# Optimization experiments

Measured on AMD Instinct MI355X. Metric: run time of the kernel, lower is better.

The kernel has to match this reference:

```python
import jax, jax.numpy as jnp
import numpy as np

EMBED_DIM = 512
NUM_HEADS = 8
HEAD_DIM = EMBED_DIM // NUM_HEADS
GRID = 48
BATCH = 8


def _locality_bias(grid_h, grid_w):
    # normalised negative squared L2 distances between patch centres, in [-1, 0]
    gy, gx = jnp.meshgrid(jnp.linspace(0.0, 1.0, grid_h),
                          jnp.linspace(0.0, 1.0, grid_w), indexing='ij')
    coords = jnp.stack([gy.reshape(-1), gx.reshape(-1)], axis=-1)  # (N, 2)
    diff = coords[None, :, :] - coords[:, None, :]                 # (N, N, 2)
    dist2 = jnp.sum(diff * diff, axis=-1)                          # (N, N)
    return -dist2 / jnp.max(dist2)


def setup_inputs() -> dict:
    key = jax.random.key(0)
    k_x, k_qkv, k_pw, k_pb, k_t, k_lw = jax.random.split(key, 6)
    N = GRID * GRID
    x = jax.random.normal(k_x, (BATCH, N, EMBED_DIM), dtype=jnp.float32)
    # torch nn.Linear weights are (out_features, in_features)
    qkv_w = jax.random.normal(k_qkv, (3 * EMBED_DIM, EMBED_DIM), dtype=jnp.float32) * 0.02
    proj_w = jax.random.normal(k_pw, (EMBED_DIM, EMBED_DIM), dtype=jnp.float32) * 0.02
    proj_b = jax.random.normal(k_pb, (EMBED_DIM,), dtype=jnp.float32) * 0.02
    init_temp = float(np.log(HEAD_DIM ** (-0.5)))
    temperature = init_temp + 0.02 * jax.random.normal(k_t, (NUM_HEADS, 1, 1), dtype=jnp.float32)
    locality_weight = 0.1 + 0.02 * jax.random.normal(k_lw, (NUM_HEADS,), dtype=jnp.float32)
    return {
        'x': x,
        'qkv_w': qkv_w,
        'proj_w': proj_w,
        'proj_b': proj_b,
        'temperature': temperature,
        'locality_weight': locality_weight,
        'grid_h': GRID,
        'grid_w': GRID,
    }


def reference(x, qkv_w, proj_w, proj_b, temperature, locality_weight, grid_h, grid_w):
    B, N, C = x.shape
    H = temperature.shape[0]
    D = C // H
    # qkv projection (no bias): (B, N, 3C) -> (3, B, H, N, D)
    qkv = (x @ qkv_w.T).reshape(B, N, 3, H, D)
    qkv = jnp.transpose(qkv, (2, 0, 3, 1, 4))
    q, k, v = qkv[0], qkv[1], qkv[2]              # each (B, H, N, D)
    scale = jnp.exp(temperature)                  # (H, 1, 1) learnable per-head temp
    attn = jnp.einsum('bhqd,bhkd->bhqk', q, k) * scale[None]
    loc = _locality_bias(grid_h, grid_w)          # (N, N), values in [-1, 0]
    attn = attn + locality_weight[None, :, None, None] * loc[None, None]
    attn = jax.nn.softmax(attn, axis=-1)          # dropout is identity (p=0 / eval)
    out = jnp.einsum('bhqk,bhkd->bhqd', attn, v)  # (B, H, N, D)
    out = jnp.transpose(out, (0, 2, 1, 3)).reshape(B, N, C)
    return out @ proj_w.T + proj_b
```

## Files before the change

### kernel.cpp

```cpp
#include <hip/hip_runtime.h>

typedef unsigned int   uint_ma   __attribute__((may_alias));
typedef unsigned short ushort_ma __attribute__((may_alias));
typedef float          float_ma  __attribute__((may_alias));
typedef __bf16 bf16x8 __attribute__((ext_vector_type(8)));
typedef float f32x4 __attribute__((ext_vector_type(4)));
typedef uint_ma u32x4 __attribute__((ext_vector_type(4)));
typedef ushort_ma u16x4 __attribute__((ext_vector_type(4)));

#define BATCH 8
#define NTOK 2304
#define CDIM 512
#define NH 8
#define HD 64
#define MROWS (BATCH * NTOK)
#define LOG2E 1.44269504088896f

constexpr size_t N_X  = (size_t)BATCH * NTOK * CDIM;
constexpr size_t N_WQ = (size_t)3 * CDIM * CDIM;
constexpr size_t N_WP = (size_t)CDIM * CDIM;
constexpr size_t OFF_XO = 0;
constexpr size_t OFF_WQ = OFF_XO + N_X;
constexpr size_t OFF_WP = OFF_WQ + N_WQ;
constexpr size_t OFF_Q  = OFF_WP + N_WP;
constexpr size_t OFF_K  = OFF_Q + N_X;
constexpr size_t OFF_V  = OFF_K + N_X;
constexpr size_t CV8 = (N_X + N_WQ + N_WP) / 8;

__device__ __forceinline__ float bf2f(unsigned short h) {
  unsigned int u = ((unsigned int)h) << 16;
  return __builtin_bit_cast(float, u);
}
__device__ __forceinline__ unsigned short f2bf(float f) {
  unsigned int u = __builtin_bit_cast(unsigned int, f);
  u += 0x7fffu + ((u >> 16) & 1u);
  return (unsigned short)(u >> 16);
}

__global__ __launch_bounds__(256) void convert3(
    const float* __restrict__ s0, const float* __restrict__ s1,
    const float* __restrict__ s2, ushort_ma* __restrict__ base) {
  const size_t gid = (size_t)blockIdx.x * blockDim.x + threadIdx.x;
  const size_t stride = (size_t)gridDim.x * blockDim.x;
  for (size_t i = gid; i < CV8; i += stride) {
    size_t r = i;
    const float* src;
    size_t doff;
    if (r < N_X / 8) { src = s0; doff = OFF_XO; }
    else if ((r -= N_X / 8) < N_WQ / 8) { src = s1; doff = OFF_WQ; }
    else { r -= N_WQ / 8; src = s2; doff = OFF_WP; }
    const f32x4* fw = (const f32x4*)(src + r * 8);
    const f32x4 a = fw[0], b = fw[1];
    u16x4 lo, hi;
#pragma unroll
    for (int j = 0; j < 4; j++) { lo[j] = f2bf(a[j]); hi[j] = f2bf(b[j]); }
    ushort_ma* dst = base + doff + r * 8;
    *(u16x4*)dst = lo;
    *(u16x4*)(dst + 4) = hi;
  }
}

template <int MODE>
__global__ __launch_bounds__(256, 2) void gemm_bt(
    const ushort_ma* __restrict__ A, const ushort_ma* __restrict__ W,
    const float* __restrict__ aux,
    unsigned short* __restrict__ o0,
    unsigned short* __restrict__ o1,
    unsigned short* __restrict__ o2)
{
  __shared__ __align__(16) ushort_ma As[128][40];
  __shared__ __align__(16) ushort_ma Bs[128][40];
  const int K = CDIM;
  const int m0 = blockIdx.x * 128;
  const int n0 = blockIdx.y * 128;
  const int t = threadIdx.x;
  const int lane = t & 63;
  const int w = t >> 6;
  const int wm = (w >> 1) * 64, wn = (w & 1) * 64;
  const int lr = lane & 15, lq = lane >> 4;

  const int ra = t >> 2;
  const int sa = (t & 3) * 8;
  const ushort_ma* Ag = A + (size_t)(m0 + ra) * K + sa;
  const ushort_ma* Ag2 = Ag + (size_t)64 * K;
  const ushort_ma* Bg = W + (size_t)(n0 + ra) * K + sa;
  const ushort_ma* Bg2 = Bg + (size_t)64 * K;

  const f32x4 fz = {0.f, 0.f, 0.f, 0.f};
  f32x4 acc[4][4];
#pragma unroll
  for (int i = 0; i < 4; i++)
#pragma unroll
    for (int j = 0; j < 4; j++) acc[i][j] = fz;

  u32x4 pa = *(const u32x4*)(Ag);
  u32x4 pa2 = *(const u32x4*)(Ag2);
  u32x4 pb = *(const u32x4*)(Bg);
  u32x4 pb2 = *(const u32x4*)(Bg2);

  for (int kt = 0; kt < 16; kt++) {
    __syncthreads();
    *(u32x4*)(&As[ra][sa]) = pa;
    *(u32x4*)(&As[ra + 64][sa]) = pa2;
    *(u32x4*)(&Bs[ra][sa]) = pb;
    *(u32x4*)(&Bs[ra + 64][sa]) = pb2;
    __syncthreads();
    if (kt < 15) {
      const int k0 = (kt + 1) * 32;
      pa = *(const u32x4*)(Ag + k0);
      pa2 = *(const u32x4*)(Ag2 + k0);
      pb = *(const u32x4*)(Bg + k0);
      pb2 = *(const u32x4*)(Bg2 + k0);
    }
    bf16x8 af[4], bfr[4];
#pragma unroll
    for (int i = 0; i < 4; i++)
      af[i] = __builtin_bit_cast(bf16x8, *(const u32x4*)(&As[wm + i * 16 + lr][lq * 8]));
#pragma unroll
    for (int j = 0; j < 4; j++)
      bfr[j] = __builtin_bit_cast(bf16x8, *(const u32x4*)(&Bs[wn + j * 16 + lr][lq * 8]));
#pragma unroll
    for (int i = 0; i < 4; i++)
#pragma unroll
      for (int j = 0; j < 4; j++)
        acc[i][j] = __builtin_amdgcn_mfma_f32_16x16x32_bf16(af[i], bfr[j], acc[i][j], 0, 0, 0);
  }

  if (MODE == 0) {
#pragma unroll
    for (int j = 0; j < 4; j++) {
      const int gc = n0 + wn + j * 16 + lr;
      const int which = gc >> 9;
      const int h = (gc >> 6) & 7;
      const int d = gc & 63;
#pragma unroll
      for (int i = 0; i < 4; i++) {
        const int gm0 = m0 + wm + i * 16 + lq * 4;
        const int b = gm0 / NTOK;
        const int np = gm0 - b * NTOK;
        if (which == 2) {
          u16x4 pk;
#pragma unroll
          for (int r = 0; r < 4; r++) pk[r] = f2bf(acc[i][j][r]);
          *(u16x4*)(o2 + ((size_t)((b * NH + h) * HD + d)) * NTOK + np) = pk;
        } else {
          const float sc = (which == 0) ? __expf(aux[h]) * LOG2E : 1.0f;
          unsigned short* dst = (which == 0) ? o0 : o1;
          const size_t base = ((size_t)((b * NH + h) * NTOK + np)) * HD + d;
#pragma unroll
          for (int r = 0; r < 4; r++) dst[base + (size_t)r * HD] = f2bf(acc[i][j][r] * sc);
        }
      }
    }
  } else {
    float_ma* outf = (float_ma*)o0;
#pragma unroll
    for (int j = 0; j < 4; j++) {
      const int gc = n0 + wn + j * 16 + lr;
      const float bv = aux[gc];
#pragma unroll
      for (int i = 0; i < 4; i++) {
        const int gm0 = m0 + wm + i * 16 + lq * 4;
#pragma unroll
        for (int r = 0; r < 4; r++)
          outf[(size_t)(gm0 + r) * CDIM + gc] = acc[i][j][r] + bv;
      }
    }
  }
}

__global__ __launch_bounds__(256, 3) void attn_kernel(
    const ushort_ma* __restrict__ Qg,
    const ushort_ma* __restrict__ Kg,
    const ushort_ma* __restrict__ Vg,
    const float* __restrict__ lwp,
    unsigned short* __restrict__ Og)
{
  __shared__ __align__(16) ushort_ma Ks[128][72];
  __shared__ __align__(16) ushort_ma Vs[64][136];
  __shared__ __align__(16) ushort_ma Ps[4][32][40];

  const int bh = blockIdx.y;
  const int b = bh >> 3, h = bh & 7;
  const int q0 = blockIdx.x * 128;
  const int t = threadIdx.x;
  const int lane = t & 63;
  const int w = t >> 6;
  const int lr = lane & 15, lq = lane >> 4;

  {
    const ushort_ma* Qb = Qg + ((size_t)bh * NTOK + q0) * HD;
#pragma unroll
    for (int it = 0; it < 4; it++) {
      const int q = t + it * 256;
      const int row = q >> 3, seg = (q & 7) * 8;
      *(u32x4*)(&Ks[row][seg]) = *(const u32x4*)(Qb + (size_t)row * HD + seg);
    }
  }
  __syncthreads();
  bf16x8 aQ[2][2];
#pragma unroll
  for (int mi = 0; mi < 2; mi++)
#pragma unroll
    for (int ks = 0; ks < 2; ks++)
      aQ[mi][ks] = __builtin_bit_cast(
          bf16x8, *(const u32x4*)(&Ks[w * 32 + mi * 16 + lr][ks * 32 + lq * 8]));

  const float cb2 = -0.5f * LOG2E * lwp[h];
  float cc[8], dd[8];
#pragma unroll
  for (int mi = 0; mi < 2; mi++)
#pragma unroll
    for (int r = 0; r < 4; r++) {
      const int qi = q0 + w * 32 + mi * 16 + lq * 4 + r;
      const int yy = qi / 48;
      const int xx = qi - yy * 48;
      cc[mi * 4 + r] = -2.0f * cb2 * ((float)yy * (1.0f / 47.0f));
      dd[mi * 4 + r] = -2.0f * cb2 * ((float)xx * (1.0f / 47.0f));
    }

  float l_i[8];
#pragma unroll
  for (int i = 0; i < 8; i++) l_i[i] = 0.0f;
  const f32x4 fz = {0.f, 0.f, 0.f, 0.f};
  f32x4 accO[2][4];
#pragma unroll
  for (int mi = 0; mi < 2; mi++)
#pragma unroll
    for (int nd = 0; nd < 4; nd++) accO[mi][nd] = fz;

  const ushort_ma* Kb = Kg + (size_t)bh * NTOK * HD;
  const ushort_ma* Vb = Vg + (size_t)bh * HD * NTOK;

  for (int kt = 0; kt < 18; kt++) {
    const int kv0 = kt * 128;
    __syncthreads();
    u32x4 kc[4], vc[4];
#pragma unroll
    for (int it = 0; it < 4; it++) {
      const int q = t + it * 256;
      kc[it] = *(const u32x4*)(Kb + (size_t)(kv0 + (q >> 3)) * HD + (q & 7) * 8);
      vc[it] = *(const u32x4*)(Vb + (size_t)(q >> 4) * NTOK + kv0 + (q & 15) * 8);
    }
#pragma unroll
    for (int it = 0; it < 4; it++) {
      const int q = t + it * 256;
      *(u32x4*)(&Ks[q >> 3][(q & 7) * 8]) = kc[it];
      *(u32x4*)(&Vs[q >> 4][(q & 15) * 8]) = vc[it];
    }
    __syncthreads();

    float ky[8], kx[8], be8[8];
#pragma unroll
    for (int ni = 0; ni < 8; ni++) {
      const int kj = kv0 + ni * 16 + lr;
      const int yy = kj / 48;
      const int xx = kj - yy * 48;
      const float fy = (float)yy * (1.0f / 47.0f);
      const float fx = (float)xx * (1.0f / 47.0f);
      ky[ni] = fy;
      kx[ni] = fx;
      be8[ni] = fmaf(cb2, fmaf(fy, fy, fx * fx), -8.0f);
    }

#pragma unroll
    for (int c = 0; c < 4; c++) {
      f32x4 s2[2][2] = {{fz, fz}, {fz, fz}};
#pragma unroll
      for (int e2 = 0; e2 < 2; e2++) {
        const int ni = 2 * c + e2;
#pragma unroll
        for (int ks = 0; ks < 2; ks++) {
          const bf16x8 bK = __builtin_bit_cast(
              bf16x8, *(const u32x4*)(&Ks[ni * 16 + lr][ks * 32 + lq * 8]));
#pragma unroll
          for (int mi = 0; mi < 2; mi++)
            s2[mi][e2] = __builtin_amdgcn_mfma_f32_16x16x32_bf16(aQ[mi][ks], bK, s2[mi][e2], 0, 0, 0);
        }
      }
#pragma unroll
      for (int e2 = 0; e2 < 2; e2++) {
        const int ni = 2 * c + e2;
        const float kyv = ky[ni], kxv = kx[ni], bev = be8[ni];
#pragma unroll
        for (int mi = 0; mi < 2; mi++)
#pragma unroll
          for (int r = 0; r < 4; r++) {
            const int ri = mi * 4 + r;
            float v = s2[mi][e2][r] + bev;
            v = fmaf(cc[ri], kyv, v);
            v = fmaf(dd[ri], kxv, v);
            const float p = __builtin_amdgcn_exp2f(v);
            const unsigned int pu = __builtin_bit_cast(unsigned int, p);
            l_i[ri] += __builtin_bit_cast(float, pu & 0xffff0000u);
            Ps[w][mi * 16 + lq * 4 + r][e2 * 16 + lr] = (unsigned short)(pu >> 16);
          }
      }
      __asm__ volatile("s_waitcnt lgkmcnt(0)" ::: "memory");
      bf16x8 aP[2];
#pragma unroll
      for (int mi = 0; mi < 2; mi++)
        aP[mi] = __builtin_bit_cast(
            bf16x8, *(const u32x4*)(&Ps[w][mi * 16 + lr][lq * 8]));
#pragma unroll
      for (int nd = 0; nd < 4; nd++) {
        const bf16x8 bV = __builtin_bit_cast(
            bf16x8, *(const u32x4*)(&Vs[nd * 16 + lr][c * 32 + lq * 8]));
#pragma unroll
        for (int mi = 0; mi < 2; mi++)
          accO[mi][nd] = __builtin_amdgcn_mfma_f32_16x16x32_bf16(aP[mi], bV, accO[mi][nd], 0, 0, 0);
      }
    }
  }

#pragma unroll
  for (int ri = 0; ri < 8; ri++) {
    float lv = l_i[ri];
    lv += __shfl_xor(lv, 1);
    lv += __shfl_xor(lv, 2);
    lv += __shfl_xor(lv, 4);
    lv += __shfl_xor(lv, 8);
    l_i[ri] = 1.0f / lv;
  }
#pragma unroll
  for (int mi = 0; mi < 2; mi++)
#pragma unroll
    for (int nd = 0; nd < 4; nd++)
#pragma unroll
      for (int r = 0; r < 4; r++) {
        const int np = q0 + w * 32 + mi * 16 + lq * 4 + r;
        Og[((size_t)(b * NTOK + np)) * CDIM + h * HD + nd * 16 + lr] =
            f2bf(accO[mi][nd][r] * l_i[mi * 4 + r]);
      }
}

extern "C" void kernel_launch(void* const* d_in, const int* in_sizes, int n_in,
                              void* d_out, int out_size, void* d_ws, size_t ws_size,
                              hipStream_t stream) {
  const float* x      = (const float*)d_in[0];
  const float* qkv_w  = (const float*)d_in[1];
  const float* proj_w = (const float*)d_in[2];
  const float* proj_b = (const float*)d_in[3];
  const float* temp   = (const float*)d_in[4];
  const float* lw     = (const float*)d_in[5];

  ushort_ma* base = (ushort_ma*)d_ws;
  ushort_ma* XB  = base + OFF_XO;
  ushort_ma* WQB = base + OFF_WQ;
  ushort_ma* WPB = base + OFF_WP;
  ushort_ma* Q   = base + OFF_Q;
  ushort_ma* Kt  = base + OFF_K;
  ushort_ma* Vt  = base + OFF_V;
  ushort_ma* O   = XB;

  convert3<<<1024, 256, 0, stream>>>(x, qkv_w, proj_w, base);
  gemm_bt<0><<<dim3(MROWS / 128, 1536 / 128), 256, 0, stream>>>(
      XB, WQB, temp, (unsigned short*)Q, (unsigned short*)Kt, (unsigned short*)Vt);
  attn_kernel<<<dim3(NTOK / 128, BATCH * NH), 256, 0, stream>>>(
      Q, Kt, Vt, lw, (unsigned short*)O);
  gemm_bt<1><<<dim3(MROWS / 128, CDIM / 128), 256, 0, stream>>>(
      O, WPB, proj_b, (unsigned short*)d_out, nullptr, nullptr);
}
```

Before: 326.0 us.

## Fold locality bias into score MFMA and use async LDS loads in GEMM

```diff
diff --git a/kernel.cpp b/kernel.cpp
--- a/kernel.cpp
+++ b/kernel.cpp
@@ -35,6 +35,12 @@
   unsigned int u = __builtin_bit_cast(unsigned int, f);
   u += 0x7fffu + ((u >> 16) & 1u);
   return (unsigned short)(u >> 16);
+}
+
+__device__ __forceinline__ void gload16(const void* g, void* l) {
+  __builtin_amdgcn_global_load_lds(
+      (const __attribute__((address_space(1))) void*)g,
+      (__attribute__((address_space(3))) void*)l, 16, 0, 0);
 }
 
 __global__ __launch_bounds__(256) void convert3(
@@ -68,8 +74,8 @@
     unsigned short* __restrict__ o1,
     unsigned short* __restrict__ o2)
 {
-  __shared__ __align__(16) ushort_ma As[128][40];
-  __shared__ __align__(16) ushort_ma Bs[128][40];
+  __shared__ __align__(16) ushort_ma As[2][128][32];
+  __shared__ __align__(16) ushort_ma Bs[2][128][32];
   const int K = CDIM;
   const int m0 = blockIdx.x * 128;
   const int n0 = blockIdx.y * 128;
@@ -79,12 +85,12 @@
   const int wm = (w >> 1) * 64, wn = (w & 1) * 64;
   const int lr = lane & 15, lq = lane >> 4;
 
-  const int ra = t >> 2;
-  const int sa = (t & 3) * 8;
-  const ushort_ma* Ag = A + (size_t)(m0 + ra) * K + sa;
-  const ushort_ma* Ag2 = Ag + (size_t)64 * K;
-  const ushort_ma* Bg = W + (size_t)(n0 + ra) * K + sa;
-  const ushort_ma* Bg2 = Bg + (size_t)64 * K;
+  const int srow = w * 16 + (lane >> 2);
+  const int scg = (lane & 3) ^ ((srow >> 1) & 3);
+  const ushort_ma* Ag0 = A + (size_t)(m0 + srow) * K + scg * 8;
+  const ushort_ma* Ag1 = Ag0 + (size_t)64 * K;
+  const ushort_ma* Bg0 = W + (size_t)(n0 + srow) * K + scg * 8;
+  const ushort_ma* Bg1 = Bg0 + (size_t)64 * K;
 
   const f32x4 fz = {0.f, 0.f, 0.f, 0.f};
   f32x4 acc[4][4];
@@ -93,32 +99,28 @@
 #pragma unroll
     for (int j = 0; j < 4; j++) acc[i][j] = fz;
 
-  u32x4 pa = *(const u32x4*)(Ag);
-  u32x4 pa2 = *(const u32x4*)(Ag2);
-  u32x4 pb = *(const u32x4*)(Bg);
-  u32x4 pb2 = *(const u32x4*)(Bg2);
+  auto issue = [&](int kt, int buf) {
+    const int k0 = kt * 32;
+    gload16(Ag0 + k0, (void*)&As[buf][w * 16][0]);
+    gload16(Ag1 + k0, (void*)&As[buf][64 + w * 16][0]);
+    gload16(Bg0 + k0, (void*)&Bs[buf][w * 16][0]);
+    gload16(Bg1 + k0, (void*)&Bs[buf][64 + w * 16][0]);
+  };
+
+  issue(0, 0);
+  const int colf = 8 * (lq ^ ((lr >> 1) & 3));
 
   for (int kt = 0; kt < 16; kt++) {
+    const int buf = kt & 1;
     __syncthreads();
-    *(u32x4*)(&As[ra][sa]) = pa;
-    *(u32x4*)(&As[ra + 64][sa]) = pa2;
-    *(u32x4*)(&Bs[ra][sa]) = pb;
-    *(u32x4*)(&Bs[ra + 64][sa]) = pb2;
-    __syncthreads();
-    if (kt < 15) {
-      const int k0 = (kt + 1) * 32;
-      pa = *(const u32x4*)(Ag + k0);
-      pa2 = *(const u32x4*)(Ag2 + k0);
-      pb = *(const u32x4*)(Bg + k0);
-      pb2 = *(const u32x4*)(Bg2 + k0);
-    }
+    if (kt < 15) issue(kt + 1, buf ^ 1);
     bf16x8 af[4], bfr[4];
 #pragma unroll
     for (int i = 0; i < 4; i++)
-      af[i] = __builtin_bit_cast(bf16x8, *(const u32x4*)(&As[wm + i * 16 + lr][lq * 8]));
+      af[i] = __builtin_bit_cast(bf16x8, *(const u32x4*)(&As[buf][wm + i * 16 + lr][colf]));
 #pragma unroll
     for (int j = 0; j < 4; j++)
-      bfr[j] = __builtin_bit_cast(bf16x8, *(const u32x4*)(&Bs[wn + j * 16 + lr][lq * 8]));
+      bfr[j] = __builtin_bit_cast(bf16x8, *(const u32x4*)(&Bs[buf][wn + j * 16 + lr][colf]));
 #pragma unroll
     for (int i = 0; i < 4; i++)
 #pragma unroll
@@ -176,7 +178,7 @@
     const float* __restrict__ lwp,
     unsigned short* __restrict__ Og)
 {
-  __shared__ __align__(16) ushort_ma Ks[128][72];
+  __shared__ __align__(16) ushort_ma Ks[128][96];
   __shared__ __align__(16) ushort_ma Vs[64][136];
   __shared__ __align__(16) ushort_ma Ps[4][32][40];
 
@@ -188,6 +190,12 @@
   const int w = t >> 6;
   const int lr = lane & 15, lq = lane >> 4;
 
+  if (t < 128) {
+    const u32x4 z4 = {0u, 0u, 0u, 0u};
+    *(u32x4*)(&Ks[t][72]) = z4;
+    *(u32x4*)(&Ks[t][80]) = z4;
+    *(u32x4*)(&Ks[t][88]) = z4;
+  }
   {
     const ushort_ma* Qb = Qg + ((size_t)bh * NTOK + q0) * HD;
 #pragma unroll
@@ -207,17 +215,21 @@
           bf16x8, *(const u32x4*)(&Ks[w * 32 + mi * 16 + lr][ks * 32 + lq * 8]));
 
   const float cb2 = -0.5f * LOG2E * lwp[h];
-  float cc[8], dd[8];
-#pragma unroll
-  for (int mi = 0; mi < 2; mi++)
-#pragma unroll
-    for (int r = 0; r < 4; r++) {
-      const int qi = q0 + w * 32 + mi * 16 + lq * 4 + r;
-      const int yy = qi / 48;
-      const int xx = qi - yy * 48;
-      cc[mi * 4 + r] = -2.0f * cb2 * ((float)yy * (1.0f / 47.0f));
-      dd[mi * 4 + r] = -2.0f * cb2 * ((float)xx * (1.0f / 47.0f));
-    }
+  bf16x8 aQb[2];
+#pragma unroll
+  for (int mi = 0; mi < 2; mi++) {
+    const int qrow = q0 + w * 32 + mi * 16 + lr;
+    const int yy = qrow / 48;
+    const int xx = qrow - yy * 48;
+    const float fy = (float)yy * (1.0f / 47.0f);
+    const float fx = (float)xx * (1.0f / 47.0f);
+    u32x4 v = {0u, 0u, 0u, 0u};
+    if (lq == 0) {
+      v[0] = (unsigned int)f2bf(fy) | ((unsigned int)f2bf(fx) << 16);
+      v[1] = (unsigned int)f2bf(fy * fy + fx * fx) | (0x3F80u << 16);
+    }
+    aQb[mi] = __builtin_bit_cast(bf16x8, v);
+  }
 
   float l_i[8];
 #pragma unroll
@@ -248,20 +260,22 @@
       *(u32x4*)(&Ks[q >> 3][(q & 7) * 8]) = kc[it];
       *(u32x4*)(&Vs[q >> 4][(q & 15) * 8]) = vc[it];
     }
-    __syncthreads();
-
-    float ky[8], kx[8], be8[8];
-#pragma unroll
-    for (int ni = 0; ni < 8; ni++) {
-      const int kj = kv0 + ni * 16 + lr;
-      const int yy = kj / 48;
-      const int xx = kj - yy * 48;
+    if (t < 128) {
+      const int kv = kv0 + t;
+      const int yy = kv / 48;
+      const int xx = kv - yy * 48;
       const float fy = (float)yy * (1.0f / 47.0f);
       const float fx = (float)xx * (1.0f / 47.0f);
-      ky[ni] = fy;
-      kx[ni] = fx;
-      be8[ni] = fmaf(cb2, fmaf(fy, fy, fx * fx), -8.0f);
-    }
+      u32x4 bv;
+      bv[0] = (unsigned int)f2bf(-2.0f * cb2 * fy) |
+              ((unsigned int)f2bf(-2.0f * cb2 * fx) << 16);
+      bv[1] = (unsigned int)f2bf(cb2) |
+              ((unsigned int)f2bf(cb2 * (fy * fy + fx * fx)) << 16);
+      bv[2] = 0u;
+      bv[3] = 0u;
+      *(u32x4*)(&Ks[t][64]) = bv;
+    }
+    __syncthreads();
 
 #pragma unroll
     for (int c = 0; c < 4; c++) {
@@ -270,27 +284,24 @@
       for (int e2 = 0; e2 < 2; e2++) {
         const int ni = 2 * c + e2;
 #pragma unroll
-        for (int ks = 0; ks < 2; ks++) {
+        for (int ks = 0; ks < 3; ks++) {
           const bf16x8 bK = __builtin_bit_cast(
               bf16x8, *(const u32x4*)(&Ks[ni * 16 + lr][ks * 32 + lq * 8]));
 #pragma unroll
-          for (int mi = 0; mi < 2; mi++)
-            s2[mi][e2] = __builtin_amdgcn_mfma_f32_16x16x32_bf16(aQ[mi][ks], bK, s2[mi][e2], 0, 0, 0);
+          for (int mi = 0; mi < 2; mi++) {
+            const bf16x8 aOp = (ks < 2) ? aQ[mi][ks] : aQb[mi];
+            s2[mi][e2] = __builtin_amdgcn_mfma_f32_16x16x32_bf16(aOp, bK, s2[mi][e2], 0, 0, 0);
+          }
         }
       }
 #pragma unroll
       for (int e2 = 0; e2 < 2; e2++) {
-        const int ni = 2 * c + e2;
-        const float kyv = ky[ni], kxv = kx[ni], bev = be8[ni];
 #pragma unroll
         for (int mi = 0; mi < 2; mi++)
 #pragma unroll
           for (int r = 0; r < 4; r++) {
             const int ri = mi * 4 + r;
-            float v = s2[mi][e2][r] + bev;
-            v = fmaf(cc[ri], kyv, v);
-            v = fmaf(dd[ri], kxv, v);
-            const float p = __builtin_amdgcn_exp2f(v);
+            const float p = __builtin_amdgcn_exp2f(s2[mi][e2][r]);
             const unsigned int pu = __builtin_bit_cast(unsigned int, p);
             l_i[ri] += __builtin_bit_cast(float, pu & 0xffff0000u);
             Ps[w][mi * 16 + lq * 4 + r][e2 * 16 + lr] = (unsigned short)(pu >> 16);
```

New measurement: 311.6 us. -4.4%, faster.
